# Kernel optimization log

Measured on AMD Instinct MI355X. Metric: run time of the kernel, lower is better.

Reference implementation:

```python
import jax, jax.numpy as jnp
import numpy as np

DIM = 1024
HEADS = 16
RADIUS = 4


def setup_inputs() -> dict:
    key = jax.random.key(0)
    ks = jax.random.split(key, 5)
    B, T, D = 4, 2048, DIM
    s = 1.0 / np.sqrt(D)
    x = jax.random.normal(ks[0], (B, T, D), dtype=jnp.float32)
    w_qkv = jax.random.uniform(ks[1], (3 * D, D), minval=-s, maxval=s, dtype=jnp.float32)
    b_qkv = jax.random.uniform(ks[2], (3 * D,), minval=-s, maxval=s, dtype=jnp.float32)
    w_proj = jax.random.uniform(ks[3], (D, D), minval=-s, maxval=s, dtype=jnp.float32)
    b_proj = jax.random.uniform(ks[4], (D,), minval=-s, maxval=s, dtype=jnp.float32)
    return {"x": x, "w_qkv": w_qkv, "b_qkv": b_qkv, "w_proj": w_proj, "b_proj": b_proj}


def reference(x, w_qkv, b_qkv, w_proj, b_proj):
    B, T, D = x.shape
    H = HEADS
    hd = D // H
    scale = hd ** -0.5
    qkv = x @ w_qkv.T + b_qkv                       # [B,T,3D]
    qkv = qkv.reshape(B, T, 3, H, hd).transpose(2, 0, 3, 1, 4)  # [3,B,H,T,hd]
    q, k, v = qkv[0], qkv[1], qkv[2]
    attn = jnp.einsum('bhqd,bhkd->bhqk', q, k) * scale  # [B,H,T,T]
    idx = jnp.arange(T)
    mask = jnp.abs(idx[None, :] - idx[:, None]) > RADIUS  # [T,T]
    attn = jnp.where(mask[None, None], -jnp.inf, attn)
    attn = jax.nn.softmax(attn, axis=-1)
    out = jnp.einsum('bhqk,bhkd->bhqd', attn, v)    # [B,H,T,hd]
    out = out.transpose(0, 2, 1, 3).reshape(B, T, D)
    return out @ w_proj.T + b_proj
```

## Files before the change

kernel.cpp:

```cpp
#include <hip/hip_runtime.h>
#include <hip/hip_bf16.h>
#include <cstdint>
#include <cstddef>
#include <type_traits>


typedef __hip_bfloat16 bf16;
typedef __attribute__((ext_vector_type(8))) short bf16x8;
typedef __attribute__((ext_vector_type(4))) float f32x4;
typedef __attribute__((ext_vector_type(8))) unsigned short u16x8;

#define BATCH  4
#define SEQ    2048
#define DIM    1024
#define NHEAD  16
#define HDIM   64
#define RADIUS 4
#define ROWS   (BATCH * SEQ)
#define KDIM   1024
#define NT     (KDIM / 64)
#define HSLICE (SEQ * HDIM)

__device__ __forceinline__ void async_copy16(const void* gptr, void* lptr) {
    __builtin_amdgcn_global_load_lds(
        (const __attribute__((address_space(1))) unsigned int*)(uintptr_t)gptr,
        (__attribute__((address_space(3))) unsigned int*)(uint32_t)(uintptr_t)lptr,
        16, 0, 0);
}

__global__ __launch_bounds__(256)
void cvt_all(const float* __restrict__ s1, bf16* __restrict__ d1, int n1,
             const float* __restrict__ s2, bf16* __restrict__ d2, int n2,
             const float* __restrict__ s3, bf16* __restrict__ d3, int n3) {
    int i = blockIdx.x * blockDim.x + threadIdx.x;
    const float* src; bf16* dst;
    if (i < n1)              { src = s1; dst = d1; }
    else if (i < n1 + n2)    { i -= n1; src = s2; dst = d2; }
    else if (i < n1+n2+n3)   { i -= n1 + n2; src = s3; dst = d3; }
    else return;
    const float4 a = ((const float4*)src)[2 * i];
    const float4 b = ((const float4*)src)[2 * i + 1];
    union { u16x8 v; __hip_bfloat16 h[8]; } o;
    o.h[0] = __float2bfloat16(a.x); o.h[1] = __float2bfloat16(a.y);
    o.h[2] = __float2bfloat16(a.z); o.h[3] = __float2bfloat16(a.w);
    o.h[4] = __float2bfloat16(b.x); o.h[5] = __float2bfloat16(b.y);
    o.h[6] = __float2bfloat16(b.z); o.h[7] = __float2bfloat16(b.w);
    ((u16x8*)dst)[i] = o.v;
}


#define BAR()        __builtin_amdgcn_s_barrier()
#define WAIT_LGKM0() asm volatile("s_waitcnt lgkmcnt(0)")

#define STAGE_A2(buf_, kt_) do {                                                \
    _Pragma("unroll")                                                           \
    for (int i_ = 0; i_ < 2; ++i_) {                                            \
        const int c_   = i_ * 512 + tid;                                        \
        const int row_ = c_ >> 3;                                               \
        const int kg_  = (c_ & 7) ^ (row_ & 7);                                 \
        async_copy16(A + (size_t)(tileM + row_) * KDIM + (kt_) + kg_ * 8,       \
                     (char*)As[buf_] + c_ * 16);                                \
    } } while (0)

#define STAGE_B3(buf_, kt_) do {                                                \
    _Pragma("unroll")                                                           \
    for (int j_ = 0; j_ < 3; ++j_) {                                            \
        const int c_   = j_ * 512 + tid;                                        \
        const int row_ = c_ >> 3;                                               \
        const int kg_  = (c_ & 7) ^ (row_ & 7);                                 \
        async_copy16(B + (size_t)(tileN + row_) * KDIM + (kt_) + kg_ * 8,       \
                     (char*)Bs[buf_] + c_ * 16);                                \
    } } while (0)

#define LDA8() do {                                                             \
    _Pragma("unroll")                                                           \
    for (int ks_ = 0; ks_ < 2; ++ks_)                                           \
    _Pragma("unroll")                                                           \
    for (int mt_ = 0; mt_ < 4; ++mt_)                                           \
        aF[ks_][mt_] = *(const bf16x8*)(as_ +                                   \
            (size_t)(wm * 64 + mt_ * 16 + l16) * 64 +                           \
            ((((ks_ << 2) | quad) ^ hh) << 3));                                 \
} while (0)

#define LDBA() do {                                                             \
    _Pragma("unroll")                                                           \
    for (int ks_ = 0; ks_ < 2; ++ks_)                                           \
    _Pragma("unroll")                                                           \
    for (int nt_ = 0; nt_ < 2; ++nt_)                                           \
        bFA[ks_][nt_] = *(const bf16x8*)(bs_ +                                  \
            (size_t)(wn * 48 + nt_ * 16 + l16) * 64 +                           \
            ((((ks_ << 2) | quad) ^ hh) << 3));                                 \
} while (0)

#define LDBB() do {                                                             \
    _Pragma("unroll")                                                           \
    for (int ks_ = 0; ks_ < 2; ++ks_)                                           \
        bFB[ks_] = *(const bf16x8*)(bs_ +                                       \
            (size_t)(wn * 48 + 32 + l16) * 64 +                                 \
            ((((ks_ << 2) | quad) ^ hh) << 3));                                 \
} while (0)

#define MFMA_N01() do {                                                         \
    _Pragma("unroll")                                                           \
    for (int ks_ = 0; ks_ < 2; ++ks_)                                           \
    _Pragma("unroll")                                                           \
    for (int mt_ = 0; mt_ < 4; ++mt_)                                           \
    _Pragma("unroll")                                                           \
    for (int nt_ = 0; nt_ < 2; ++nt_)                                           \
        acc[mt_][nt_] = __builtin_amdgcn_mfma_f32_16x16x32_bf16(                \
            aF[ks_][mt_], bFA[ks_][nt_], acc[mt_][nt_], 0, 0, 0);               \
} while (0)

#define MFMA_N2() do {                                                          \
    _Pragma("unroll")                                                           \
    for (int ks_ = 0; ks_ < 2; ++ks_)                                           \
    _Pragma("unroll")                                                           \
    for (int mt_ = 0; mt_ < 4; ++mt_)                                           \
        acc[mt_][2] = __builtin_amdgcn_mfma_f32_16x16x32_bf16(                  \
            aF[ks_][mt_], bFB[ks_], acc[mt_][2], 0, 0, 0);                      \
} while (0)

__global__ __launch_bounds__(512, 4)
void gemm_qkv_2b(const bf16* __restrict__ A, const bf16* __restrict__ B,
                 const float* __restrict__ bias, bf16* __restrict__ C) {
    __shared__ bf16 As[2][128 * 64];
    __shared__ bf16 Bs[2][192 * 64];

    const int tid  = threadIdx.x;
    const int l16  = tid & 15;
    const int quad = (tid >> 4) & 3;
    const int wave = tid >> 6;
    const int wm   = wave >> 2;
    const int wn   = wave & 3;
    const int hh   = l16 & 7;

    const int bid = (int)blockIdx.x;
    const int seq = (bid & 7) * 128 + (bid >> 3);
    const int tileM = (seq >> 4) * 128;
    const int tileN = (seq & 15) * 192;

    f32x4  acc[4][3] = {};
    bf16x8 aF[2][4], bFA[2][2], bFB[2];

    STAGE_A2(0, 0);  STAGE_B3(0, 0);  STAGE_A2(1, 64);
    asm volatile("s_waitcnt vmcnt(2)" ::: "memory");
    BAR();

    #pragma unroll 1
    for (int t = 0; t < NT; ++t) {
        const int buf = t & 1;
        const bf16* __restrict__ as_ = &As[buf][0];
        const bf16* __restrict__ bs_ = &Bs[buf][0];

        LDA8();
        LDBA();
        if (t + 1 < NT) STAGE_B3(buf ^ 1, (t + 1) * 64);
        asm volatile("s_waitcnt lgkmcnt(8)");
        BAR();
        WAIT_LGKM0();
        __builtin_amdgcn_s_setprio(1);
        MFMA_N01();
        __builtin_amdgcn_s_setprio(0);
        BAR();

        LDBB();
        if (t + 2 < NT) STAGE_A2(buf, (t + 2) * 64);
        BAR();
        WAIT_LGKM0();
        __builtin_amdgcn_s_setprio(1);
        MFMA_N2();
        __builtin_amdgcn_s_setprio(0);
        if (t + 2 < NT)         asm volatile("s_waitcnt vmcnt(2)" ::: "memory");
        else if (t + 1 < NT)    asm volatile("s_waitcnt vmcnt(0)" ::: "memory");
        BAR();
    }

    float  bvs[3];
    size_t cbase[3];
    #pragma unroll
    for (int an = 0; an < 3; ++an) {
        const int cl = tileN + wn * 48 + an * 16 + l16;
        bvs[an] = bias[cl];
        const int s = cl >> 10;
        const int h = (cl >> 6) & (NHEAD - 1);
        const int d = cl & 63;
        cbase[an] = (size_t)(h * 3 + s) * HSLICE + d;
    }
    #pragma unroll
    for (int mt = 0; mt < 4; ++mt) {
        #pragma unroll
        for (int r = 0; r < 4; ++r) {
            const int rowg = tileM + wm * 64 + mt * 16 + quad * 4 + r;
            const int b  = rowg >> 11;
            const int tt = rowg & (SEQ - 1);
            const size_t rb = (size_t)b * (NHEAD * 3) * HSLICE + (size_t)tt * HDIM;
            #pragma unroll
            for (int an = 0; an < 3; ++an)
                C[rb + cbase[an]] = __float2bfloat16(acc[mt][an][r] + bvs[an]);
        }
    }
}

template <int NMAT, typename OutT>
__device__ __forceinline__
void gemm_body(const bf16* __restrict__ A, const bf16* __restrict__ B,
               const float* __restrict__ bias, OutT* __restrict__ C) {
    __shared__ bf16 As[128 * 64];
    __shared__ bf16 Bs[128 * 64];

    const int tid  = threadIdx.x;
    const int lane = tid & 63;
    const int wave = tid >> 6;
    const int quad = lane >> 4;
    const int l16  = lane & 15;

    const int tileM = blockIdx.y * 128;
    const int tileN = blockIdx.x * 128;
    const int wm = (wave >> 1) * 64;
    const int wn = (wave & 1) * 64;

    f32x4 acc[4][4] = {};

    for (int kt = 0; kt < KDIM; kt += 64) {
        #pragma unroll
        for (int i = 0; i < 4; ++i) {
            const int c   = i * 256 + tid;
            const int row = c >> 3;
            const int kg  = (c & 7) ^ (row & 7);
            async_copy16(A + (size_t)(tileM + row) * KDIM + kt + kg * 8,
                         (char*)As + c * 16);
            async_copy16(B + (size_t)(tileN + row) * KDIM + kt + kg * 8,
                         (char*)Bs + c * 16);
        }
        __syncthreads();

        #pragma unroll
        for (int ks = 0; ks < 2; ++ks) {
            const int kq = ks * 4 + quad;
            const int so = (kq ^ (l16 & 7)) * 8;
            bf16x8 aF[4], bF[4];
            #pragma unroll
            for (int mt = 0; mt < 4; ++mt)
                aF[mt] = *(const bf16x8*)(As + (wm + mt * 16 + l16) * 64 + so);
            #pragma unroll
            for (int nt = 0; nt < 4; ++nt)
                bF[nt] = *(const bf16x8*)(Bs + (wn + nt * 16 + l16) * 64 + so);

            #pragma unroll
            for (int mt = 0; mt < 4; ++mt)
                #pragma unroll
                for (int nt = 0; nt < 4; ++nt)
                    acc[mt][nt] = __builtin_amdgcn_mfma_f32_16x16x32_bf16(
                        aF[mt], bF[nt], acc[mt][nt], 0, 0, 0);
        }
        __syncthreads();
    }

    #pragma unroll
    for (int nt = 0; nt < 4; ++nt) {
        const int scol = tileN + wn + nt * 16;
        const float bv = bias[scol + l16];
        #pragma unroll
        for (int mt = 0; mt < 4; ++mt) {
            #pragma unroll
            for (int r = 0; r < 4; ++r) {
                const int rowg = tileM + wm + mt * 16 + quad * 4 + r;
                const float v = acc[mt][nt][r] + bv;
                C[(size_t)rowg * NMAT + scol + l16] = v;
            }
        }
    }
}

__global__ __launch_bounds__(256)
void gemm_proj(const bf16* __restrict__ A, const bf16* __restrict__ B,
               const float* __restrict__ bias, float* __restrict__ C) {
    gemm_body<1024, float>(A, B, bias, C);
}

__device__ __forceinline__ void bf8_to_f32(const uint4 u, float* f) {
    union { uint32_t u; float f; } c;
    c.u = u.x << 16;         f[0] = c.f;
    c.u = u.x & 0xffff0000u; f[1] = c.f;
    c.u = u.y << 16;         f[2] = c.f;
    c.u = u.y & 0xffff0000u; f[3] = c.f;
    c.u = u.z << 16;         f[4] = c.f;
    c.u = u.z & 0xffff0000u; f[5] = c.f;
    c.u = u.w << 16;         f[6] = c.f;
    c.u = u.w & 0xffff0000u; f[7] = c.f;
}

__global__ __launch_bounds__(256)
void attn_banded4(const bf16* __restrict__ qkv, bf16* __restrict__ aout) {
    const int tid = threadIdx.x;
    const int qi  = tid >> 2;
    const int ch  = tid & 3;
    const int t   = blockIdx.x * 64 + qi;
    const int h   = blockIdx.y;
    const int b   = blockIdx.z;

    const size_t bh3 = (size_t)(b * NHEAD + h) * 3;
    const bf16* qb = qkv + (bh3 + 0) * HSLICE + (size_t)t * HDIM + ch * 16;
    const bf16* kb = qkv + (bh3 + 1) * HSLICE + ch * 16;
    const bf16* vb = qkv + (bh3 + 2) * HSLICE + ch * 16;
    const float scale = 0.125f;

    float q16[16];
    {
        const uint4* qp = (const uint4*)qb;
        uint4 u0 = qp[0], u1 = qp[1];
        bf8_to_f32(u0, q16); bf8_to_f32(u1, q16 + 8);
    }

    float sc[2 * RADIUS + 1];
    #pragma unroll
    for (int j = 0; j < 2 * RADIUS + 1; ++j) {
        const int k = t - RADIUS + j;
        const bool valid = (k >= 0) && (k < SEQ);
        const int kc = valid ? k : t;
        const uint4* kp = (const uint4*)(kb + (size_t)kc * HDIM);
        float kf[16];
        uint4 u0 = kp[0], u1 = kp[1];
        bf8_to_f32(u0, kf); bf8_to_f32(u1, kf + 8);
        float p = 0.f;
        #pragma unroll
        for (int e = 0; e < 16; ++e) p = fmaf(q16[e], kf[e], p);
        p += __shfl_xor(p, 1, 64);
        p += __shfl_xor(p, 2, 64);
        sc[j] = valid ? p * scale : -1e30f;
    }

    float mx = sc[0];
    #pragma unroll
    for (int j = 1; j < 2 * RADIUS + 1; ++j) mx = fmaxf(mx, sc[j]);
    float sum = 0.f;
    #pragma unroll
    for (int j = 0; j < 2 * RADIUS + 1; ++j) { sc[j] = __expf(sc[j] - mx); sum += sc[j]; }
    const float inv = 1.0f / sum;

    float o16[16];
    #pragma unroll
    for (int e = 0; e < 16; ++e) o16[e] = 0.f;
    #pragma unroll
    for (int j = 0; j < 2 * RADIUS + 1; ++j) {
        const int k = t - RADIUS + j;
        const int kc = (k >= 0 && k < SEQ) ? k : t;
        const uint4* vp = (const uint4*)(vb + (size_t)kc * HDIM);
        float vf[16];
        uint4 u0 = vp[0], u1 = vp[1];
        bf8_to_f32(u0, vf); bf8_to_f32(u1, vf + 8);
        const float w = sc[j];
        #pragma unroll
        for (int e = 0; e < 16; ++e) o16[e] = fmaf(w, vf[e], o16[e]);
    }

    bf16* op = aout + ((size_t)b * SEQ + t) * DIM + h * HDIM + ch * 16;
    #pragma unroll
    for (int c2 = 0; c2 < 2; ++c2) {
        union { u16x8 v; __hip_bfloat16 hh[8]; } o;
        #pragma unroll
        for (int e = 0; e < 8; ++e) o.hh[e] = __float2bfloat16(o16[c2 * 8 + e] * inv);
        ((u16x8*)op)[c2] = o.v;
    }
}

extern "C" void kernel_launch(void* const* d_in, const int* in_sizes, int n_in,
                              void* d_out, int out_size, void* d_ws, size_t ws_size,
                              hipStream_t stream) {
    const float* x      = (const float*)d_in[0];
    const float* w_qkv  = (const float*)d_in[1];
    const float* b_qkv  = (const float*)d_in[2];
    const float* w_proj = (const float*)d_in[3];
    const float* b_proj = (const float*)d_in[4];
    float* out = (float*)d_out;

    bf16* xb     = (bf16*)d_ws;
    bf16* wqkvb  = xb + (size_t)ROWS * DIM;
    bf16* wprojb = wqkvb + (size_t)3072 * 1024;
    bf16* qkvb   = wprojb + (size_t)1024 * 1024;
    bf16* attnb  = qkvb + (size_t)ROWS * 3072;

    const int n1 = ROWS * DIM / 8, n2 = 3072 * 1024 / 8, n3 = 1024 * 1024 / 8;
    cvt_all<<<(n1 + n2 + n3 + 255) / 256, 256, 0, stream>>>(x, xb, n1, w_qkv, wqkvb, n2,
                                                            w_proj, wprojb, n3);

    gemm_qkv_2b<<<dim3(1024), 512, 0, stream>>>(xb, wqkvb, b_qkv, qkvb);

    attn_banded4<<<dim3(SEQ / 64, NHEAD, BATCH), 256, 0, stream>>>(qkvb, attnb);

    gemm_proj<<<dim3(1024 / 128, ROWS / 128), 256, 0, stream>>>(attnb, wprojb, b_proj, out);
}
```

Measured before the change: 191.7 us.

## Rewrite projection GEMM with double-buffered async loads and 8-wave blocks

Replaces the simple single-buffered 256-thread projection GEMM with a 512-thread, double-buffered version modeled on the QKV GEMM. Global-to-LDS loads for the next K tile are interleaved with the MFMA phases, using split barriers, vmcnt waits and s_setprio. It also remaps block IDs for tile locality. This is meant to hide memory latency and raise MFMA utilisation, at the cost of twice the LDS per block and more intricate synchronisation.

```diff
diff --git a/kernel.cpp b/kernel.cpp
--- a/kernel.cpp
+++ b/kernel.cpp
@@ -48,9 +48,9 @@
     ((u16x8*)dst)[i] = o.v;
 }
 
-
 #define BAR()        __builtin_amdgcn_s_barrier()
 #define WAIT_LGKM0() asm volatile("s_waitcnt lgkmcnt(0)")
+
 
 #define STAGE_A2(buf_, kt_) do {                                                \
     _Pragma("unroll")                                                           \
@@ -201,81 +201,122 @@
     }
 }
 
-template <int NMAT, typename OutT>
-__device__ __forceinline__
-void gemm_body(const bf16* __restrict__ A, const bf16* __restrict__ B,
-               const float* __restrict__ bias, OutT* __restrict__ C) {
-    __shared__ bf16 As[128 * 64];
-    __shared__ bf16 Bs[128 * 64];
+
+#define STAGE_AP(buf_, kt_) do {                                                \
+    _Pragma("unroll")                                                           \
+    for (int i_ = 0; i_ < 2; ++i_) {                                            \
+        const int c_   = i_ * 512 + tid;                                        \
+        const int row_ = c_ >> 3;                                               \
+        const int kg_  = (c_ & 7) ^ (row_ & 7);                                 \
+        async_copy16(A + (size_t)(tileM + row_) * KDIM + (kt_) + kg_ * 8,       \
+                     (char*)Ap[buf_] + c_ * 16);                                \
+    } } while (0)
+
+#define STAGE_BP(buf_, kt_) do {                                                \
+    _Pragma("unroll")                                                           \
+    for (int i_ = 0; i_ < 2; ++i_) {                                            \
+        const int c_   = i_ * 512 + tid;                                        \
+        const int row_ = c_ >> 3;                                               \
+        const int kg_  = (c_ & 7) ^ (row_ & 7);                                 \
+        async_copy16(B + (size_t)(tileN + row_) * KDIM + (kt_) + kg_ * 8,       \
+                     (char*)Bp[buf_] + c_ * 16);                                \
+    } } while (0)
+
+#define LDAP() do {                                                             \
+    _Pragma("unroll")                                                           \
+    for (int ks_ = 0; ks_ < 2; ++ks_)                                           \
+    _Pragma("unroll")                                                           \
+    for (int mt_ = 0; mt_ < 4; ++mt_)                                           \
+        aF[ks_][mt_] = *(const bf16x8*)(as_ +                                   \
+            (size_t)(wm * 64 + mt_ * 16 + l16) * 64 +                           \
+            ((((ks_ << 2) | quad) ^ hh) << 3));                                 \
+} while (0)
+
+#define LDBP(reg_, nt_) do {                                                    \
+    _Pragma("unroll")                                                           \
+    for (int ks_ = 0; ks_ < 2; ++ks_)                                           \
+        reg_[ks_] = *(const bf16x8*)(bs_ +                                      \
+            (size_t)(wn * 32 + (nt_) * 16 + l16) * 64 +                         \
+            ((((ks_ << 2) | quad) ^ hh) << 3));                                 \
+} while (0)
+
+#define MFMA_P(nt_, reg_) do {                                                  \
+    _Pragma("unroll")                                                           \
+    for (int ks_ = 0; ks_ < 2; ++ks_)                                           \
+    _Pragma("unroll")                                                           \
+    for (int mt_ = 0; mt_ < 4; ++mt_)                                           \
+        acc[mt_][nt_] = __builtin_amdgcn_mfma_f32_16x16x32_bf16(                \
+            aF[ks_][mt_], reg_[ks_], acc[mt_][nt_], 0, 0, 0);                   \
+} while (0)
+
+__global__ __launch_bounds__(512, 4)
+void gemm_proj_2b(const bf16* __restrict__ A, const bf16* __restrict__ B,
+                  const float* __restrict__ bias, float* __restrict__ C) {
+    __shared__ bf16 Ap[2][128 * 64];
+    __shared__ bf16 Bp[2][128 * 64];
 
     const int tid  = threadIdx.x;
-    const int lane = tid & 63;
+    const int l16  = tid & 15;
+    const int quad = (tid >> 4) & 3;
     const int wave = tid >> 6;
-    const int quad = lane >> 4;
-    const int l16  = lane & 15;
-
-    const int tileM = blockIdx.y * 128;
-    const int tileN = blockIdx.x * 128;
-    const int wm = (wave >> 1) * 64;
-    const int wn = (wave & 1) * 64;
-
-    f32x4 acc[4][4] = {};
-
-    for (int kt = 0; kt < KDIM; kt += 64) {
+    const int wm   = wave >> 2;
+    const int wn   = wave & 3;
+    const int hh   = l16 & 7;
+
+    const int bid = (int)blockIdx.x;
+    const int seq = (bid & 7) * 64 + (bid >> 3);
+    const int tileM = (seq >> 3) * 128;
+    const int tileN = (seq & 7) * 128;
+
+    f32x4  acc[4][2] = {};
+    bf16x8 aF[2][4], bF0[2], bF1[2];
+
+    STAGE_AP(0, 0);  STAGE_BP(0, 0);  STAGE_AP(1, 64);
+    asm volatile("s_waitcnt vmcnt(2)" ::: "memory");
+    BAR();
+
+    #pragma unroll 1
+    for (int t = 0; t < NT; ++t) {
+        const int buf = t & 1;
+        const bf16* __restrict__ as_ = &Ap[buf][0];
+        const bf16* __restrict__ bs_ = &Bp[buf][0];
+
+        LDAP();
+        LDBP(bF0, 0);
+        if (t + 1 < NT) STAGE_BP(buf ^ 1, (t + 1) * 64);
+        asm volatile("s_waitcnt lgkmcnt(8)");
+        BAR();
+        WAIT_LGKM0();
+        __builtin_amdgcn_s_setprio(1);
+        MFMA_P(0, bF0);
+        __builtin_amdgcn_s_setprio(0);
+        BAR();
+
+        LDBP(bF1, 1);
+        if (t + 2 < NT) STAGE_AP(buf, (t + 2) * 64);
+        BAR();
+        WAIT_LGKM0();
+        __builtin_amdgcn_s_setprio(1);
+        MFMA_P(1, bF1);
+        __builtin_amdgcn_s_setprio(0);
+        if (t + 2 < NT)         asm volatile("s_waitcnt vmcnt(2)" ::: "memory");
+        else if (t + 1 < NT)    asm volatile("s_waitcnt vmcnt(0)" ::: "memory");
+        BAR();
+    }
+
+    float bvs[2];
+    #pragma unroll
+    for (int nt = 0; nt < 2; ++nt) bvs[nt] = bias[tileN + wn * 32 + nt * 16 + l16];
+    #pragma unroll
+    for (int mt = 0; mt < 4; ++mt) {
         #pragma unroll
-        for (int i = 0; i < 4; ++i) {
-            const int c   = i * 256 + tid;
-            const int row = c >> 3;
-            const int kg  = (c & 7) ^ (row & 7);
-            async_copy16(A + (size_t)(tileM + row) * KDIM + kt + kg * 8,
-                         (char*)As + c * 16);
-            async_copy16(B + (size_t)(tileN + row) * KDIM + kt + kg * 8,
-                         (char*)Bs + c * 16);
+        for (int r = 0; r < 4; ++r) {
+            const int rowg = tileM + wm * 64 + mt * 16 + quad * 4 + r;
+            float* cp = C + (size_t)rowg * DIM + tileN + wn * 32 + l16;
+            cp[0]  = acc[mt][0][r] + bvs[0];
+            cp[16] = acc[mt][1][r] + bvs[1];
         }
-        __syncthreads();
-
-        #pragma unroll
-        for (int ks = 0; ks < 2; ++ks) {
-            const int kq = ks * 4 + quad;
-            const int so = (kq ^ (l16 & 7)) * 8;
-            bf16x8 aF[4], bF[4];
-            #pragma unroll
-            for (int mt = 0; mt < 4; ++mt)
-                aF[mt] = *(const bf16x8*)(As + (wm + mt * 16 + l16) * 64 + so);
-            #pragma unroll
-            for (int nt = 0; nt < 4; ++nt)
-                bF[nt] = *(const bf16x8*)(Bs + (wn + nt * 16 + l16) * 64 + so);
-
-            #pragma unroll
-            for (int mt = 0; mt < 4; ++mt)
-                #pragma unroll
-                for (int nt = 0; nt < 4; ++nt)
-                    acc[mt][nt] = __builtin_amdgcn_mfma_f32_16x16x32_bf16(
-                        aF[mt], bF[nt], acc[mt][nt], 0, 0, 0);
-        }
-        __syncthreads();
-    }
-
-    #pragma unroll
-    for (int nt = 0; nt < 4; ++nt) {
-        const int scol = tileN + wn + nt * 16;
-        const float bv = bias[scol + l16];
-        #pragma unroll
-        for (int mt = 0; mt < 4; ++mt) {
-            #pragma unroll
-            for (int r = 0; r < 4; ++r) {
-                const int rowg = tileM + wm + mt * 16 + quad * 4 + r;
-                const float v = acc[mt][nt][r] + bv;
-                C[(size_t)rowg * NMAT + scol + l16] = v;
-            }
-        }
-    }
-}
-
-__global__ __launch_bounds__(256)
-void gemm_proj(const bf16* __restrict__ A, const bf16* __restrict__ B,
-               const float* __restrict__ bias, float* __restrict__ C) {
-    gemm_body<1024, float>(A, B, bias, C);
+    }
 }
 
 __device__ __forceinline__ void bf8_to_f32(const uint4 u, float* f) {
@@ -388,5 +429,5 @@
 
     attn_banded4<<<dim3(SEQ / 64, NHEAD, BATCH), 256, 0, stream>>>(qkvb, attnb);
 
-    gemm_proj<<<dim3(1024 / 128, ROWS / 128), 256, 0, stream>>>(attnb, wprojb, b_proj, out);
-}
+    gemm_proj_2b<<<dim3(512), 512, 0, stream>>>(attnb, wprojb, b_proj, out);
+}
```

After: 187.1 us. -2.4%, faster.
